# Performance work log

Measured on AMD Instinct MI355X. Metric: run time of the kernel, lower is better.

The kernel has to match this reference:

```python
import jax, jax.numpy as jnp
import numpy as np

N_HEADS = 16
DIM_HEAD = 64
ROPE_THETA = 10000.0


def _rope_tables(seq_len, dim_head, dtype):
    # [N, dim_head//2] angle tables, llama-style interleaved-pair rotation
    inv_freq = 1.0 / (ROPE_THETA ** (jnp.arange(0, dim_head, 2, dtype=jnp.float32) / dim_head))
    t = jnp.arange(seq_len, dtype=jnp.float32)
    freqs = jnp.outer(t, inv_freq)  # [N, D/2]
    return jnp.cos(freqs).astype(dtype), jnp.sin(freqs).astype(dtype)


def _apply_rope(x, cos, sin):
    # x: [B, H, N, D]; rotate interleaved pairs (x[2i], x[2i+1])
    xr = x[..., 0::2]
    xi = x[..., 1::2]
    cos = cos[None, None, :, :]
    sin = sin[None, None, :, :]
    out_r = xr * cos - xi * sin
    out_i = xr * sin + xi * cos
    return jnp.stack([out_r, out_i], axis=-1).reshape(x.shape)


def _l2norm(x, eps=1e-12):
    return x / jnp.maximum(jnp.linalg.norm(x, axis=-1, keepdims=True), eps)


def setup_inputs() -> dict:
    key = jax.random.key(0)
    ks = jax.random.split(key, 5)
    B, N, dim = 1, 4096, N_HEADS * DIM_HEAD
    q = jax.random.normal(ks[0], (B, N, dim), dtype=jnp.float32)
    k = jax.random.normal(ks[1], (B, N, dim), dtype=jnp.float32)
    v = jax.random.normal(ks[2], (B, N, dim), dtype=jnp.float32)
    qk_scale = jnp.full((1, 1, 1, DIM_HEAD), 10.0, dtype=jnp.float32)
    w_out = jax.random.normal(ks[3], (dim, dim), dtype=jnp.float32) * (dim ** -0.5)
    b_out = jnp.zeros((dim,), dtype=jnp.float32)
    return {"q": q, "k": k, "v": v, "qk_scale": qk_scale, "w_out": w_out, "b_out": b_out}


def reference(q, k, v, qk_scale, w_out, b_out):
    B, N, dim = q.shape
    H, D = N_HEADS, DIM_HEAD
    scale = D ** -0.5
    # [B, N, dim] -> [B, H, N, D]
    q = q.reshape(B, N, H, D).transpose(0, 2, 1, 3)
    k = k.reshape(B, N, H, D).transpose(0, 2, 1, 3)
    v = v.reshape(B, N, H, D).transpose(0, 2, 1, 3)
    # RoPE
    cos, sin = _rope_tables(N, D, q.dtype)
    q = _apply_rope(q, cos, sin)
    k = _apply_rope(k, cos, sin)
    # QK-norm: L2-normalize then learned scale
    q = _l2norm(q) * qk_scale
    k = _l2norm(k) * qk_scale
    # explicit attention (non-flash)
    scores = jnp.einsum('bhid,bhjd->bhij', q, k) * scale
    probs = jax.nn.softmax(scores, axis=-1)
    out = jnp.einsum('bhij,bhjd->bhid', probs, v)
    out = out.transpose(0, 2, 1, 3).reshape(B, N, dim)
    # Linear: y = x W^T + b
    return out @ w_out.T + b_out
```

## Files before the change

kernel.cpp:

```cpp
#include <hip/hip_runtime.h>
#include <hip/hip_bf16.h>

#define N_CTX 4096
#define NH    16
#define DH    64
#define DIM   1024
#define NSPLIT 2
#define KT_PER_SPLIT (N_CTX / 64 / NSPLIT)

typedef __attribute__((ext_vector_type(8))) short bf16x8;
typedef __attribute__((ext_vector_type(4))) float f32x4;

__device__ __forceinline__ ushort f2bf(float f) {
    union { float f; unsigned u; } x; x.f = f;
    unsigned r = (x.u + 0x7FFFu + ((x.u >> 16) & 1u)) >> 16;
    return (ushort)r;
}
__device__ __forceinline__ float bf2f(ushort u) {
    union { unsigned u; float f; } x; x.u = ((unsigned)u) << 16; return x.f;
}
__device__ __forceinline__ unsigned fbits(float f) {
    union { float f; unsigned u; } x; x.f = f; return x.u;
}
__device__ __forceinline__ unsigned pack_bf16(float lo, float hi) {
    unsigned a = fbits(lo) + 0x8000u;
    unsigned b = fbits(hi) + 0x8000u;
#if defined(__has_builtin)
#if __has_builtin(__builtin_amdgcn_perm)
    return __builtin_amdgcn_perm(b, a, 0x07060302u);
#else
    return (a >> 16) | (b & 0xFFFF0000u);
#endif
#else
    return (a >> 16) | (b & 0xFFFF0000u);
#endif
}
__device__ __forceinline__ float fast_exp2(float x) {
#if defined(__has_builtin)
#if __has_builtin(__builtin_amdgcn_exp2f)
    return __builtin_amdgcn_exp2f(x);
#else
    return exp2f(x);
#endif
#else
    return exp2f(x);
#endif
}
__device__ __forceinline__ void fast_sincos(float ang, float* s, float* c) {
#if defined(__has_builtin)
#if __has_builtin(__builtin_amdgcn_sinf) && __has_builtin(__builtin_amdgcn_cosf) && __has_builtin(__builtin_amdgcn_fractf)
    float rev = __builtin_amdgcn_fractf(ang * 0.15915494309189535f);
    *s = __builtin_amdgcn_sinf(rev);
    *c = __builtin_amdgcn_cosf(rev);
    return;
#endif
#endif
    sincosf(ang, s, c);
}

#define SC 0.18033688011112042f
#define LF 0.4152410118609203f

__global__ __launch_bounds__(256) void prep_kernel(
    const float* __restrict__ qg, const float* __restrict__ kg,
    const float* __restrict__ qk_scale,
    ushort* __restrict__ qb, ushort* __restrict__ kb)
{
    const int lane = threadIdx.x & 63;
    const int wave = threadIdx.x >> 6;
    const int row  = blockIdx.x * 4 + wave;
    const int n = row >> 4;
    const int h = row & 15;
    const int isk = blockIdx.y;
    const float* __restrict__ x = isk ? kg : qg;
    ushort* __restrict__ xb = isk ? kb : qb;
    const float premul = isk ? 1.0f : SC;

    float val = x[(size_t)n * DIM + h * DH + lane];
    float other = __shfl_xor(val, 1, 64);

    const int i = lane >> 1;
    float inv_freq = fast_exp2((float)i * -LF);
    float ang = (float)n * inv_freq;
    float s, c;
    fast_sincos(ang, &s, &c);

    float r = (lane & 1) ? fmaf(other, s, val * c)
                         : fmaf(val, c, -(other * s));

    float ss = r * r;
    #pragma unroll
    for (int off = 32; off > 0; off >>= 1)
        ss += __shfl_xor(ss, off, 64);
    float invn = rsqrtf(fmaxf(ss, 1e-24f));
    float scl  = qk_scale[lane] * premul;

    xb[((size_t)h * N_CTX + n) * DH + lane] = f2bf(r * invn * scl);
}

__global__ __launch_bounds__(256) void vtrans_kernel(
    const float* __restrict__ v, ushort* __restrict__ vt)
{
    __shared__ ushort L[64][68];
    const int kt = blockIdx.x, h = blockIdx.y, t = threadIdx.x;

    for (int e = t; e < 4096; e += 256) {
        int key = e >> 6, d = e & 63;
        float f = v[(size_t)(kt * 64 + key) * DIM + h * DH + d];
        L[d][key] = f2bf(f);
    }
    __syncthreads();
    for (int e = t; e < 4096; e += 256) {
        int d = e >> 6, key = e & 63;
        vt[((size_t)h * DH + d) * N_CTX + kt * 64 + key] = L[d][key];
    }
}

__global__ __launch_bounds__(256) void wconv_kernel(
    const float* __restrict__ w, ushort* __restrict__ wb)
{
    int i = (blockIdx.x * 256 + threadIdx.x) * 4;
    float4 f = *(const float4*)&w[i];
    ushort4 u;
    u.x = f2bf(f.x); u.y = f2bf(f.y); u.z = f2bf(f.z); u.w = f2bf(f.w);
    *(ushort4*)&wb[i] = u;
}

__global__ __launch_bounds__(256) void attn_kernel(
    const ushort* __restrict__ qb, const ushort* __restrict__ kb,
    const ushort* __restrict__ vt, ushort* __restrict__ opart,
    float* __restrict__ lpart)
{
    __shared__ ushort Ks[64][72];
    __shared__ ushort Vt[64][72];
    __shared__ ushort Ps[128][72];

    const int h     = blockIdx.y;
    const int qbase = blockIdx.x * 128;
    const int sp    = blockIdx.z;
    const int kbase = sp * (N_CTX / NSPLIT);
    const int t    = threadIdx.x;
    const int w    = t >> 6;
    const int lane = t & 63;
    const int l15  = lane & 15;
    const int quad = lane >> 4;

    bf16x8 qf[2][2];
    #pragma unroll
    for (int qt = 0; qt < 2; qt++) {
        const size_t qrow = ((size_t)h * N_CTX + qbase + w * 32 + qt * 16 + l15) * DH;
        qf[qt][0] = *(const bf16x8*)&qb[qrow + quad * 8];
        qf[qt][1] = *(const bf16x8*)&qb[qrow + 32 + quad * 8];
    }

    float l_part[2] = {0.0f, 0.0f};
    f32x4 o_acc[4][2];
    #pragma unroll
    for (int dt = 0; dt < 4; dt++)
        #pragma unroll
        for (int qt = 0; qt < 2; qt++)
            o_acc[dt][qt] = (f32x4){0.f, 0.f, 0.f, 0.f};

    const int sr = t >> 3;
    const int sc = (t & 7) * 8;
    const ushort* kp0 = &kb[((size_t)h * N_CTX + kbase + sr) * DH + sc];
    const ushort* kp1 = kp0 + (size_t)32 * DH;
    const ushort* vp0 = &vt[((size_t)h * DH + sr) * N_CTX + kbase + sc];
    const ushort* vp1 = vp0 + (size_t)32 * N_CTX;
    bf16x8 kr0 = *(const bf16x8*)kp0, kr1 = *(const bf16x8*)kp1;
    bf16x8 vr0 = *(const bf16x8*)vp0, vr1 = *(const bf16x8*)vp1;

    for (int kt = 0; kt < KT_PER_SPLIT; kt++) {
        __syncthreads();
        *(bf16x8*)&Ks[sr][sc]      = kr0;
        *(bf16x8*)&Ks[sr + 32][sc] = kr1;
        *(bf16x8*)&Vt[sr][sc]      = vr0;
        *(bf16x8*)&Vt[sr + 32][sc] = vr1;
        __syncthreads();
        if (kt + 1 < KT_PER_SPLIT) {
            kr0 = *(const bf16x8*)(kp0 + (size_t)(kt + 1) * 64 * DH);
            kr1 = *(const bf16x8*)(kp1 + (size_t)(kt + 1) * 64 * DH);
            vr0 = *(const bf16x8*)(vp0 + (size_t)(kt + 1) * 64);
            vr1 = *(const bf16x8*)(vp1 + (size_t)(kt + 1) * 64);
        }

        #pragma unroll
        for (int j = 0; j < 4; j++) {
            bf16x8 kf0 = *(const bf16x8*)&Ks[j * 16 + l15][quad * 8];
            bf16x8 kf1 = *(const bf16x8*)&Ks[j * 16 + l15][32 + quad * 8];
            f32x4 s0 = (f32x4){0.f, 0.f, 0.f, 0.f};
            f32x4 s1 = (f32x4){0.f, 0.f, 0.f, 0.f};
            s0 = __builtin_amdgcn_mfma_f32_16x16x32_bf16(kf0, qf[0][0], s0, 0, 0, 0);
            s1 = __builtin_amdgcn_mfma_f32_16x16x32_bf16(kf0, qf[1][0], s1, 0, 0, 0);
            s0 = __builtin_amdgcn_mfma_f32_16x16x32_bf16(kf1, qf[0][1], s0, 0, 0, 0);
            s1 = __builtin_amdgcn_mfma_f32_16x16x32_bf16(kf1, qf[1][1], s1, 0, 0, 0);

            {
                float p0 = fast_exp2(s0.x), p1 = fast_exp2(s0.y);
                float p2 = fast_exp2(s0.z), p3 = fast_exp2(s0.w);
                l_part[0] += (p0 + p1) + (p2 + p3);
                uint2 pk; pk.x = pack_bf16(p0, p1); pk.y = pack_bf16(p2, p3);
                *(uint2*)&Ps[w * 32 + l15][j * 16 + quad * 4] = pk;
            }
            {
                float p0 = fast_exp2(s1.x), p1 = fast_exp2(s1.y);
                float p2 = fast_exp2(s1.z), p3 = fast_exp2(s1.w);
                l_part[1] += (p0 + p1) + (p2 + p3);
                uint2 pk; pk.x = pack_bf16(p0, p1); pk.y = pack_bf16(p2, p3);
                *(uint2*)&Ps[w * 32 + 16 + l15][j * 16 + quad * 4] = pk;
            }
        }

        #pragma unroll
        for (int ks = 0; ks < 2; ks++) {
            bf16x8 pf0 = *(const bf16x8*)&Ps[w * 32 + l15][ks * 32 + quad * 8];
            bf16x8 pf1 = *(const bf16x8*)&Ps[w * 32 + 16 + l15][ks * 32 + quad * 8];
            #pragma unroll
            for (int dt = 0; dt < 4; dt++) {
                bf16x8 vf = *(const bf16x8*)&Vt[dt * 16 + l15][ks * 32 + quad * 8];
                o_acc[dt][0] = __builtin_amdgcn_mfma_f32_16x16x32_bf16(vf, pf0, o_acc[dt][0], 0, 0, 0);
                o_acc[dt][1] = __builtin_amdgcn_mfma_f32_16x16x32_bf16(vf, pf1, o_acc[dt][1], 0, 0, 0);
            }
        }
    }

    #pragma unroll
    for (int qt = 0; qt < 2; qt++) {
        float v = l_part[qt];
        v += __shfl_xor(v, 16, 64);
        v += __shfl_xor(v, 32, 64);
        if (quad == 0)
            lpart[(size_t)sp * NH * N_CTX + (size_t)h * N_CTX
                  + qbase + w * 32 + qt * 16 + l15] = v;
    }

    #pragma unroll
    for (int qt = 0; qt < 2; qt++)
        #pragma unroll
        for (int dt = 0; dt < 4; dt++) {
            f32x4 o = o_acc[dt][qt];
            ushort4 ov;
            ov.x = f2bf(o.x); ov.y = f2bf(o.y);
            ov.z = f2bf(o.z); ov.w = f2bf(o.w);
            *(ushort4*)&opart[((size_t)sp * N_CTX + qbase + w * 32 + qt * 16 + l15) * DIM
                              + h * DH + dt * 16 + quad * 4] = ov;
        }
}

__global__ __launch_bounds__(256) void combine_kernel(
    const ushort* __restrict__ opart, const float* __restrict__ lpart,
    ushort* __restrict__ attnb)
{
    const int idx = blockIdx.x * 256 + threadIdx.x;
    const int n   = idx >> 8;
    const int rem = idx & 255;
    const int h   = rem >> 4;
    const size_t e = (size_t)n * DIM + h * DH + (rem & 15) * 4;

    float s0 = 0.f, s1 = 0.f, s2 = 0.f, s3 = 0.f, lsum = 0.f;
    #pragma unroll
    for (int sp = 0; sp < NSPLIT; sp++) {
        ushort4 u = *(const ushort4*)&opart[(size_t)sp * N_CTX * DIM + e];
        s0 += bf2f(u.x); s1 += bf2f(u.y); s2 += bf2f(u.z); s3 += bf2f(u.w);
        lsum += lpart[(size_t)sp * NH * N_CTX + (size_t)h * N_CTX + n];
    }
    float li = 1.0f / lsum;

    ushort4 r;
    r.x = f2bf(s0 * li); r.y = f2bf(s1 * li);
    r.z = f2bf(s2 * li); r.w = f2bf(s3 * li);
    *(ushort4*)&attnb[e] = r;
}

__global__ __launch_bounds__(256) void proj_kernel(
    const ushort* __restrict__ A, const ushort* __restrict__ W,
    const float* __restrict__ bias, float* __restrict__ out)
{
    __shared__ ushort As[64][72];
    __shared__ ushort Ws[64][72];

    const int nbase = blockIdx.x * 64;
    const int obase = blockIdx.y * 64;
    const int t    = threadIdx.x;
    const int w    = t >> 6;
    const int lane = t & 63;
    const int l15  = lane & 15;
    const int quad = lane >> 4;
    const int rw   = (w >> 1) * 32;
    const int cw   = (w & 1) * 32;

    f32x4 acc[2][2];
    #pragma unroll
    for (int mt = 0; mt < 2; mt++)
        #pragma unroll
        for (int nt = 0; nt < 2; nt++)
            acc[mt][nt] = (f32x4){0.f, 0.f, 0.f, 0.f};

    for (int kt = 0; kt < DIM / 64; kt++) {
        const int kb = kt * 64;
        __syncthreads();
        #pragma unroll
        for (int i = 0; i < 2; i++) {
            int c = t + i * 256, r = c >> 3, c8 = c & 7;
            *(bf16x8*)&As[r][c8 * 8] =
                *(const bf16x8*)&A[(size_t)(nbase + r) * DIM + kb + c8 * 8];
        }
        #pragma unroll
        for (int i = 0; i < 2; i++) {
            int c = t + i * 256, r = c >> 3, c8 = c & 7;
            *(bf16x8*)&Ws[r][c8 * 8] =
                *(const bf16x8*)&W[(size_t)(obase + r) * DIM + kb + c8 * 8];
        }
        __syncthreads();

        bf16x8 af[2][2], bfr[2][2];
        #pragma unroll
        for (int mt = 0; mt < 2; mt++)
            #pragma unroll
            for (int kh = 0; kh < 2; kh++)
                af[mt][kh] = *(const bf16x8*)&As[rw + mt * 16 + l15][kh * 32 + quad * 8];
        #pragma unroll
        for (int nt = 0; nt < 2; nt++)
            #pragma unroll
            for (int kh = 0; kh < 2; kh++)
                bfr[nt][kh] = *(const bf16x8*)&Ws[cw + nt * 16 + l15][kh * 32 + quad * 8];

        #pragma unroll
        for (int mt = 0; mt < 2; mt++)
            #pragma unroll
            for (int nt = 0; nt < 2; nt++) {
                acc[mt][nt] = __builtin_amdgcn_mfma_f32_16x16x32_bf16(af[mt][0], bfr[nt][0], acc[mt][nt], 0, 0, 0);
                acc[mt][nt] = __builtin_amdgcn_mfma_f32_16x16x32_bf16(af[mt][1], bfr[nt][1], acc[mt][nt], 0, 0, 0);
            }
    }

    #pragma unroll
    for (int nt = 0; nt < 2; nt++) {
        int o = obase + cw + nt * 16 + l15;
        float bb = bias[o];
        #pragma unroll
        for (int mt = 0; mt < 2; mt++) {
            int nrow = nbase + rw + mt * 16 + quad * 4;
            out[(size_t)(nrow + 0) * DIM + o] = acc[mt][nt].x + bb;
            out[(size_t)(nrow + 1) * DIM + o] = acc[mt][nt].y + bb;
            out[(size_t)(nrow + 2) * DIM + o] = acc[mt][nt].z + bb;
            out[(size_t)(nrow + 3) * DIM + o] = acc[mt][nt].w + bb;
        }
    }
}

extern "C" void kernel_launch(void* const* d_in, const int* in_sizes, int n_in,
                              void* d_out, int out_size, void* d_ws, size_t ws_size,
                              hipStream_t stream)
{
    const float* q        = (const float*)d_in[0];
    const float* k        = (const float*)d_in[1];
    const float* v        = (const float*)d_in[2];
    const float* qk_scale = (const float*)d_in[3];
    const float* w_out    = (const float*)d_in[4];
    const float* b_out    = (const float*)d_in[5];
    float* out = (float*)d_out;

    const size_t per = (size_t)NH * N_CTX * DH;
    ushort* qb    = (ushort*)d_ws;
    ushort* kb    = qb + per;
    ushort* vtg   = kb + per;
    ushort* attnb = vtg + per;
    ushort* wb    = attnb + per;
    ushort* opart = wb + (size_t)DIM * DIM;
    float*  lpart = (float*)(opart + (size_t)NSPLIT * N_CTX * DIM);

    prep_kernel<<<dim3(N_CTX * NH / 4, 2), 256, 0, stream>>>(q, k, qk_scale, qb, kb);
    vtrans_kernel<<<dim3(N_CTX / 64, NH), 256, 0, stream>>>(v, vtg);
    wconv_kernel<<<dim3(DIM * DIM / 1024), 256, 0, stream>>>(w_out, wb);
    attn_kernel<<<dim3(N_CTX / 128, NH, NSPLIT), 256, 0, stream>>>(qb, kb, vtg, opart, lpart);
    combine_kernel<<<dim3(N_CTX * DIM / 4 / 256), 256, 0, stream>>>(opart, lpart, attnb);
    proj_kernel<<<dim3(N_CTX / 64, DIM / 64), 256, 0, stream>>>(attnb, wb, b_out, out);
}
```

Before: 232.9 us.

## Fuse split-combine into projection loads and merge V/W conversion kernels

Removes the separate combine kernel: the projection GEMM now reads both split partial outputs, sums them, normalizes by the combined softmax denominator and packs to bf16 while staging its A tile. The V-transpose and weight-conversion kernels are merged into one launch with block-index dispatch. This cuts two launches and a full intermediate write/read of the attention output. The cost is that the combine work is redone for every output-column block of the projection (16x redundant opart reads and math). The lpart indexing uses kt as the head index, which matches because each 64-wide K tile corresponds to one head.

```diff
diff --git a/kernel.cpp b/kernel.cpp
--- a/kernel.cpp
+++ b/kernel.cpp
@@ -98,32 +98,32 @@
     xb[((size_t)h * N_CTX + n) * DH + lane] = f2bf(r * invn * scl);
 }
 
-__global__ __launch_bounds__(256) void vtrans_kernel(
-    const float* __restrict__ v, ushort* __restrict__ vt)
+__global__ __launch_bounds__(256) void vw_kernel(
+    const float* __restrict__ v, ushort* __restrict__ vt,
+    const float* __restrict__ w, ushort* __restrict__ wb)
 {
     __shared__ ushort L[64][68];
-    const int kt = blockIdx.x, h = blockIdx.y, t = threadIdx.x;
-
-    for (int e = t; e < 4096; e += 256) {
-        int key = e >> 6, d = e & 63;
-        float f = v[(size_t)(kt * 64 + key) * DIM + h * DH + d];
-        L[d][key] = f2bf(f);
-    }
-    __syncthreads();
-    for (int e = t; e < 4096; e += 256) {
-        int d = e >> 6, key = e & 63;
-        vt[((size_t)h * DH + d) * N_CTX + kt * 64 + key] = L[d][key];
-    }
-}
-
-__global__ __launch_bounds__(256) void wconv_kernel(
-    const float* __restrict__ w, ushort* __restrict__ wb)
-{
-    int i = (blockIdx.x * 256 + threadIdx.x) * 4;
-    float4 f = *(const float4*)&w[i];
-    ushort4 u;
-    u.x = f2bf(f.x); u.y = f2bf(f.y); u.z = f2bf(f.z); u.w = f2bf(f.w);
-    *(ushort4*)&wb[i] = u;
+    const int bx = blockIdx.x, t = threadIdx.x;
+
+    if (bx < 1024) {
+        const int kt = bx & 63, h = bx >> 6;
+        for (int e = t; e < 4096; e += 256) {
+            int key = e >> 6, d = e & 63;
+            float f = v[(size_t)(kt * 64 + key) * DIM + h * DH + d];
+            L[d][key] = f2bf(f);
+        }
+        __syncthreads();
+        for (int e = t; e < 4096; e += 256) {
+            int d = e >> 6, key = e & 63;
+            vt[((size_t)h * DH + d) * N_CTX + kt * 64 + key] = L[d][key];
+        }
+    } else {
+        int i = ((bx - 1024) * 256 + t) * 4;
+        float4 f = *(const float4*)&w[i];
+        ushort4 u;
+        u.x = f2bf(f.x); u.y = f2bf(f.y); u.z = f2bf(f.z); u.w = f2bf(f.w);
+        *(ushort4*)&wb[i] = u;
+    }
 }
 
 __global__ __launch_bounds__(256) void attn_kernel(
@@ -247,34 +247,10 @@
         }
 }
 
-__global__ __launch_bounds__(256) void combine_kernel(
+__global__ __launch_bounds__(256) void proj_kernel(
     const ushort* __restrict__ opart, const float* __restrict__ lpart,
-    ushort* __restrict__ attnb)
-{
-    const int idx = blockIdx.x * 256 + threadIdx.x;
-    const int n   = idx >> 8;
-    const int rem = idx & 255;
-    const int h   = rem >> 4;
-    const size_t e = (size_t)n * DIM + h * DH + (rem & 15) * 4;
-
-    float s0 = 0.f, s1 = 0.f, s2 = 0.f, s3 = 0.f, lsum = 0.f;
-    #pragma unroll
-    for (int sp = 0; sp < NSPLIT; sp++) {
-        ushort4 u = *(const ushort4*)&opart[(size_t)sp * N_CTX * DIM + e];
-        s0 += bf2f(u.x); s1 += bf2f(u.y); s2 += bf2f(u.z); s3 += bf2f(u.w);
-        lsum += lpart[(size_t)sp * NH * N_CTX + (size_t)h * N_CTX + n];
-    }
-    float li = 1.0f / lsum;
-
-    ushort4 r;
-    r.x = f2bf(s0 * li); r.y = f2bf(s1 * li);
-    r.z = f2bf(s2 * li); r.w = f2bf(s3 * li);
-    *(ushort4*)&attnb[e] = r;
-}
-
-__global__ __launch_bounds__(256) void proj_kernel(
-    const ushort* __restrict__ A, const ushort* __restrict__ W,
-    const float* __restrict__ bias, float* __restrict__ out)
+    const ushort* __restrict__ W, const float* __restrict__ bias,
+    float* __restrict__ out)
 {
     __shared__ ushort As[64][72];
     __shared__ ushort Ws[64][72];
@@ -302,8 +278,29 @@
         #pragma unroll
         for (int i = 0; i < 2; i++) {
             int c = t + i * 256, r = c >> 3, c8 = c & 7;
-            *(bf16x8*)&As[r][c8 * 8] =
-                *(const bf16x8*)&A[(size_t)(nbase + r) * DIM + kb + c8 * 8];
+            int n = nbase + r;
+            float li = 1.0f / (lpart[(size_t)kt * N_CTX + n]
+                             + lpart[(size_t)NH * N_CTX + (size_t)kt * N_CTX + n]);
+            const size_t e = (size_t)n * DIM + kb + c8 * 8;
+            bf16x8 u0 = *(const bf16x8*)&opart[e];
+            bf16x8 u1 = *(const bf16x8*)&opart[(size_t)N_CTX * DIM + e];
+            uint2 pk;
+            {
+                float a0 = (bf2f((ushort)u0[0]) + bf2f((ushort)u1[0])) * li;
+                float a1 = (bf2f((ushort)u0[1]) + bf2f((ushort)u1[1])) * li;
+                float a2 = (bf2f((ushort)u0[2]) + bf2f((ushort)u1[2])) * li;
+                float a3 = (bf2f((ushort)u0[3]) + bf2f((ushort)u1[3])) * li;
+                pk.x = pack_bf16(a0, a1); pk.y = pack_bf16(a2, a3);
+                *(uint2*)&As[r][c8 * 8] = pk;
+            }
+            {
+                float a0 = (bf2f((ushort)u0[4]) + bf2f((ushort)u1[4])) * li;
+                float a1 = (bf2f((ushort)u0[5]) + bf2f((ushort)u1[5])) * li;
+                float a2 = (bf2f((ushort)u0[6]) + bf2f((ushort)u1[6])) * li;
+                float a3 = (bf2f((ushort)u0[7]) + bf2f((ushort)u1[7])) * li;
+                pk.x = pack_bf16(a0, a1); pk.y = pack_bf16(a2, a3);
+                *(uint2*)&As[r][c8 * 8 + 4] = pk;
+            }
         }
         #pragma unroll
         for (int i = 0; i < 2; i++) {
@@ -365,15 +362,12 @@
     ushort* qb    = (ushort*)d_ws;
     ushort* kb    = qb + per;
     ushort* vtg   = kb + per;
-    ushort* attnb = vtg + per;
-    ushort* wb    = attnb + per;
+    ushort* wb    = vtg + per;
     ushort* opart = wb + (size_t)DIM * DIM;
     float*  lpart = (float*)(opart + (size_t)NSPLIT * N_CTX * DIM);
 
     prep_kernel<<<dim3(N_CTX * NH / 4, 2), 256, 0, stream>>>(q, k, qk_scale, qb, kb);
-    vtrans_kernel<<<dim3(N_CTX / 64, NH), 256, 0, stream>>>(v, vtg);
-    wconv_kernel<<<dim3(DIM * DIM / 1024), 256, 0, stream>>>(w_out, wb);
+    vw_kernel<<<dim3(1024 + DIM * DIM / 1024), 256, 0, stream>>>(v, vtg, w_out, wb);
     attn_kernel<<<dim3(N_CTX / 128, NH, NSPLIT), 256, 0, stream>>>(qb, kb, vtg, opart, lpart);
-    combine_kernel<<<dim3(N_CTX * DIM / 4 / 256), 256, 0, stream>>>(opart, lpart, attnb);
-    proj_kernel<<<dim3(N_CTX / 64, DIM / 64), 256, 0, stream>>>(attnb, wb, b_out, out);
-}
+    proj_kernel<<<dim3(N_CTX / 64, DIM / 64), 256, 0, stream>>>(opart, lpart, wb, b_out, out);
+}
```

Result: slower. 238.1 us (+2.2%).
